# Performance work log

Measured on AMD Instinct MI355X. Metric: run time of the kernel, lower is better.

The kernel has to match this reference:

```python
import jax, jax.numpy as jnp
import numpy as np

N_NODES = 50000
N_EDGES = 1600000
IN_DIM = 128
HID = 128
N_GRAPHS = 64
N_CLASSES = 1


def _seg_sum(x, ids, n):
    return jax.ops.segment_sum(x, ids, num_segments=n)


def _gcn_layer(h, W, b, src, dst, src_isqrt, dst_isqrt):
    # DGL GraphConv, norm='both': D_dst^{-1/2} A D_src^{-1/2} (h W) + b
    hw = h @ W                                  # [N, out]
    msg = (hw * src_isqrt[:, None])[src]        # gather -> [E, out]
    agg = _seg_sum(msg, dst, h.shape[0])        # scatter-add -> [N, out]
    return agg * dst_isqrt[:, None] + b


def setup_inputs() -> dict:
    key = jax.random.key(0)
    ks = jax.random.split(key, 16)
    x = jax.random.normal(ks[0], (N_NODES, IN_DIM), dtype=jnp.float32)
    src = jax.random.randint(ks[1], (N_EDGES,), 0, N_NODES)
    dst = jax.random.randint(ks[2], (N_EDGES,), 0, N_NODES)
    graph_id = jnp.sort(jax.random.randint(ks[3], (N_NODES,), 0, N_GRAPHS))
    s = 1.0 / np.sqrt(HID)
    params = {
        'W1': jax.random.uniform(ks[4], (IN_DIM, HID), jnp.float32, -s, s),
        'b1': jnp.zeros((HID,), jnp.float32),
        'W2': jax.random.uniform(ks[5], (HID, HID), jnp.float32, -s, s),
        'b2': jnp.zeros((HID,), jnp.float32),
        'Wc1': jax.random.uniform(ks[6], (HID, HID // 2), jnp.float32, -s, s),
        'bc1': jnp.zeros((HID // 2,), jnp.float32),
        'Wc2': jax.random.uniform(ks[7], (HID // 2, HID // 4), jnp.float32, -s, s),
        'bc2': jnp.zeros((HID // 4,), jnp.float32),
        'Wc3': jax.random.uniform(ks[8], (HID // 4, HID // 8), jnp.float32, -s, s),
        'bc3': jnp.zeros((HID // 8,), jnp.float32),
        'Wc4': jax.random.uniform(ks[9], (HID // 8, N_CLASSES), jnp.float32, -s, s),
        'bc4': jnp.zeros((N_CLASSES,), jnp.float32),
    }
    return dict(x=x, src=src, dst=dst, graph_id=graph_id, num_graphs=N_GRAPHS, **params)


def reference(x, src, dst, graph_id, num_graphs, W1, b1, W2, b2,
              Wc1, bc1, Wc2, bc2, Wc3, bc3, Wc4, bc4):
    n = x.shape[0]
    ones = jnp.ones((src.shape[0],), x.dtype)
    out_deg = jnp.clip(_seg_sum(ones, src, n), 1.0)
    in_deg = jnp.clip(_seg_sum(ones, dst, n), 1.0)
    src_isqrt = jax.lax.rsqrt(out_deg)
    dst_isqrt = jax.lax.rsqrt(in_deg)

    h = jax.nn.relu(_gcn_layer(x, W1, b1, src, dst, src_isqrt, dst_isqrt))
    h = jax.nn.relu(_gcn_layer(h, W2, b2, src, dst, src_isqrt, dst_isqrt))

    # dgl.mean_nodes: per-graph mean of node features
    sums = _seg_sum(h, graph_id, num_graphs)                       # [G, HID]
    cnts = jnp.clip(_seg_sum(jnp.ones((n,), h.dtype), graph_id, num_graphs), 1.0)
    hg = sums / cnts[:, None]

    o = jax.nn.relu(hg @ Wc1 + bc1)
    o = jax.nn.relu(o @ Wc2 + bc2)
    o = jax.nn.relu(o @ Wc3 + bc3)
    return o @ Wc4 + bc4
```

## Files before the change

### kernel.cpp

```cpp
#include <hip/hip_runtime.h>
#include <hip/hip_fp16.h>

#define FDIM 128
#define NGRAPH 64
#define CBLK 256

typedef _Float16 f16;
typedef f16 f16x8 __attribute__((ext_vector_type(8)));
typedef float f32x4 __attribute__((ext_vector_type(4)));
typedef float f32x2 __attribute__((ext_vector_type(2)));

__device__ __forceinline__ int lower_bound_i(const int* a, int n, int v) {
    int lo = 0, hi = n;
    while (lo < hi) { int m = (lo + hi) >> 1; if (a[m] < v) lo = m + 1; else hi = m; }
    return lo;
}

__global__ __launch_bounds__(256) void k_pre(
        const float* __restrict__ W1, f16* __restrict__ W1h, f16* __restrict__ W1l,
        const float* __restrict__ W2, f16* __restrict__ W2h, f16* __restrict__ W2l,
        float* __restrict__ hg, const int* __restrict__ src, const int* __restrict__ dst,
        int* __restrict__ out_deg, int* __restrict__ partial,
        int E, int NBIN, int CE4) {
    __shared__ int lds[4 * 257];
    const int t = threadIdx.x;
    int b = blockIdx.x;
    if (b < 128) {
        int i = b * 256 + t;
        if (i < NGRAPH * FDIM) hg[i] = 0.f;
        int j = i & 16383;
        int k = j >> 7, n = j & 127;
        const float* W = (i < 16384) ? W1 : W2;
        f16* Wh = (i < 16384) ? W1h : W2h;
        f16* Wl = (i < 16384) ? W1l : W2l;
        float v = W[j];
        f16 hi = (f16)v;
        Wh[n * FDIM + k] = hi;
        Wl[n * FDIM + k] = (f16)(v - (float)hi);
    } else {
        b -= 128;
        for (int i = t; i < 4 * 257; i += 256) lds[i] = 0;
        __syncthreads();
        const int wv = t >> 6;
        int* hh = &lds[wv * 257];
        const int s = b * CE4, e = min(E, s + CE4);
        for (int i = s + t * 4; i < e; i += 1024) {
            if (i + 4 <= e) {
                uint4 d4 = *(const uint4*)&dst[i];
                uint4 s4 = *(const uint4*)&src[i];
                atomicAdd(&hh[d4.x >> 8], 1);
                atomicAdd(&hh[d4.y >> 8], 1);
                atomicAdd(&hh[d4.z >> 8], 1);
                atomicAdd(&hh[d4.w >> 8], 1);
                atomicAdd(&out_deg[s4.x], 1);
                atomicAdd(&out_deg[s4.y], 1);
                atomicAdd(&out_deg[s4.z], 1);
                atomicAdd(&out_deg[s4.w], 1);
            } else {
                for (int j = i; j < e; j++) {
                    atomicAdd(&hh[dst[j] >> 8], 1);
                    atomicAdd(&out_deg[src[j]], 1);
                }
            }
        }
        __syncthreads();
        for (int i = t; i < NBIN; i += 256)
            partial[i * CBLK + b] = lds[i] + lds[257 + i] + lds[514 + i] + lds[771 + i];
    }
}

__global__ __launch_bounds__(256) void k_scan(
        const int* __restrict__ partial, int* __restrict__ offs, int* __restrict__ bsum,
        int M) {
    __shared__ int lds[256];
    const int t = threadIdx.x;
    const int b = blockIdx.x;
    int i = b * 256 + t;
    int v = (i < M) ? partial[i] : 0;
    lds[t] = v;
    __syncthreads();
    for (int off = 1; off < 256; off <<= 1) {
        int x = (t >= off) ? lds[t - off] : 0;
        __syncthreads();
        lds[t] += x;
        __syncthreads();
    }
    if (i < M) offs[i] = lds[t] - v;
    if (t == 255) bsum[b] = lds[t];
}

__global__ __launch_bounds__(256) void k_coarse_scatter(
        const int* __restrict__ src, const int* __restrict__ dst,
        const int* __restrict__ offs, const int* __restrict__ bsum,
        unsigned* __restrict__ coarse_buf, int E, int CE4, int NBIN) {
    __shared__ int cur[256], sb[256];
    const int t = threadIdx.x, b = blockIdx.x;
    int v = (t < NBIN) ? bsum[t] : 0;
    sb[t] = v;
    __syncthreads();
    for (int off = 1; off < 256; off <<= 1) {
        int x = (t >= off) ? sb[t - off] : 0;
        __syncthreads();
        sb[t] += x;
        __syncthreads();
    }
    if (t < NBIN) cur[t] = offs[t * CBLK + b] + (sb[t] - v);
    __syncthreads();
    const int s = b * CE4, e = min(E, s + CE4);
    for (int i = s + t * 4; i < e; i += 1024) {
        if (i + 4 <= e) {
            uint4 d4 = *(const uint4*)&dst[i];
            uint4 s4 = *(const uint4*)&src[i];
            int p0 = atomicAdd(&cur[d4.x >> 8], 1);
            int p1 = atomicAdd(&cur[d4.y >> 8], 1);
            int p2 = atomicAdd(&cur[d4.z >> 8], 1);
            int p3 = atomicAdd(&cur[d4.w >> 8], 1);
            coarse_buf[p0] = (d4.x << 16) | s4.x;
            coarse_buf[p1] = (d4.y << 16) | s4.y;
            coarse_buf[p2] = (d4.z << 16) | s4.z;
            coarse_buf[p3] = (d4.w << 16) | s4.w;
        } else {
            for (int j = i; j < e; j++) {
                unsigned d = (unsigned)dst[j];
                int p = atomicAdd(&cur[d >> 8], 1);
                coarse_buf[p] = (d << 16) | (unsigned)src[j];
            }
        }
    }
}

template<bool IN_F16>
__device__ __forceinline__ void gemm_body(
        f16* smem, float* sisql, int blk,
        const void* __restrict__ Xv, const f16* __restrict__ Wh,
        const f16* __restrict__ Wl, const int* __restrict__ out_deg,
        float* __restrict__ sisq, unsigned char* __restrict__ out, int N) {
    const int t = threadIdx.x;
    const int w = t >> 6;
    const int lane = t & 63;
    const int base = blk * 128;

    if (t < 128) {
        int row = base + t;
        float sv = 1.f;
        if (row < N) {
            if (IN_F16) {
                sv = sisq[row];
            } else {
                sv = rsqrtf((float)max(out_deg[row], 1));
                sisq[row] = sv;
            }
        }
        sisql[t] = sv;
    }
    for (int i = t; i < 2048; i += 256) {
        int n = i >> 4, kc = (i & 15) * 8;
        *(uint4*)&smem[n * 136 + kc] = *(const uint4*)&Wh[n * FDIM + kc];
    }
    __syncthreads();

    const int mrow = lane & 15;
    const int kq = (lane >> 4) * 8;
    const int arow0 = min(base + w * 32 + mrow, N - 1);
    const int arow1 = min(base + w * 32 + 16 + mrow, N - 1);

    f16x8 a0[4], a1[4];
    if (IN_F16) {
        const f16* X = (const f16*)Xv;
#pragma unroll
        for (int kk = 0; kk < 4; kk++) {
            a0[kk] = *(const f16x8*)&X[(size_t)arow0 * FDIM + kk * 32 + kq];
            a1[kk] = *(const f16x8*)&X[(size_t)arow1 * FDIM + kk * 32 + kq];
        }
    } else {
        const float* X = (const float*)Xv;
#pragma unroll
        for (int kk = 0; kk < 4; kk++) {
            float4 u0 = *(const float4*)&X[(size_t)arow0 * FDIM + kk * 32 + kq];
            float4 u1 = *(const float4*)&X[(size_t)arow0 * FDIM + kk * 32 + kq + 4];
            float4 v0 = *(const float4*)&X[(size_t)arow1 * FDIM + kk * 32 + kq];
            float4 v1 = *(const float4*)&X[(size_t)arow1 * FDIM + kk * 32 + kq + 4];
            f16x8 av;
            av[0] = (f16)u0.x; av[1] = (f16)u0.y; av[2] = (f16)u0.z; av[3] = (f16)u0.w;
            av[4] = (f16)u1.x; av[5] = (f16)u1.y; av[6] = (f16)u1.z; av[7] = (f16)u1.w;
            a0[kk] = av;
            av[0] = (f16)v0.x; av[1] = (f16)v0.y; av[2] = (f16)v0.z; av[3] = (f16)v0.w;
            av[4] = (f16)v1.x; av[5] = (f16)v1.y; av[6] = (f16)v1.z; av[7] = (f16)v1.w;
            a1[kk] = av;
        }
    }

    f32x4 acc0[8], acc1[8];
#pragma unroll
    for (int nt = 0; nt < 8; nt++) {
        acc0[nt] = (f32x4){0.f, 0.f, 0.f, 0.f};
        acc1[nt] = (f32x4){0.f, 0.f, 0.f, 0.f};
    }

#pragma unroll
    for (int kk = 0; kk < 4; kk++) {
#pragma unroll
        for (int nt = 0; nt < 8; nt++) {
            f16x8 bh = *(const f16x8*)&smem[(nt * 16 + mrow) * 136 + kk * 32 + kq];
            f16x8 bl = *(const f16x8*)&Wl[(nt * 16 + mrow) * FDIM + kk * 32 + kq];
            acc0[nt] = __builtin_amdgcn_mfma_f32_16x16x32_f16(a0[kk], bh, acc0[nt], 0, 0, 0);
            acc1[nt] = __builtin_amdgcn_mfma_f32_16x16x32_f16(a1[kk], bh, acc1[nt], 0, 0, 0);
            acc0[nt] = __builtin_amdgcn_mfma_f32_16x16x32_f16(a0[kk], bl, acc0[nt], 0, 0, 0);
            acc1[nt] = __builtin_amdgcn_mfma_f32_16x16x32_f16(a1[kk], bl, acc1[nt], 0, 0, 0);
        }
    }

    const int r0 = (lane >> 4) * 4;
    float sv0[4], sv1[4];
#pragma unroll
    for (int j = 0; j < 4; j++) {
        sv0[j] = sisql[w * 32 + r0 + j];
        sv1[j] = sisql[w * 32 + 16 + r0 + j];
    }
    __syncthreads();
#pragma unroll
    for (int nt = 0; nt < 8; nt++) {
        int c = nt * 16 + mrow;
#pragma unroll
        for (int j = 0; j < 4; j++) {
            smem[(w * 32 + r0 + j) * 136 + c]      = (f16)(acc0[nt][j] * sv0[j]);
            smem[(w * 32 + 16 + r0 + j) * 136 + c] = (f16)(acc1[nt][j] * sv1[j]);
        }
    }
    __syncthreads();
    {
        int r = t >> 1, cb = (t & 1) * 64;
        int row = base + r;
        if (row < N) {
            unsigned char* dstp = out + (size_t)row * FDIM + cb;
#pragma unroll
            for (int g2 = 0; g2 < 4; g2++) {
                unsigned wv[4];
#pragma unroll
                for (int k2 = 0; k2 < 4; k2++) {
                    const f16* p = &smem[r * 136 + cb + g2 * 16 + k2 * 4];
                    int w0 = __builtin_amdgcn_cvt_pk_fp8_f32((float)p[0], (float)p[1], 0, false);
                    w0 = __builtin_amdgcn_cvt_pk_fp8_f32((float)p[2], (float)p[3], w0, true);
                    wv[k2] = (unsigned)w0;
                }
                uint4 u;
                u.x = wv[0]; u.y = wv[1]; u.z = wv[2]; u.w = wv[3];
                *(uint4*)&dstp[g2 * 16] = u;
            }
        }
    }
}

__global__ __launch_bounds__(256) void k_fine_gemm(
        const unsigned* __restrict__ coarse_buf, const int* __restrict__ bsum,
        int* __restrict__ csr_src, int* __restrict__ row_ptr, int N, int E, int NBIN,
        const float* __restrict__ x, const f16* __restrict__ Wh,
        const f16* __restrict__ Wl, const int* __restrict__ out_deg,
        float* __restrict__ sisq, unsigned char* __restrict__ hws) {
    __shared__ __align__(16) f16 smem[128 * 136];
    __shared__ float sisql[128];
    const int t = threadIdx.x;
    const int g = blockIdx.x;
    if (g >= NBIN) {
        gemm_body<false>(smem, sisql, g - NBIN, x, Wh, Wl, out_deg, sisq, hws, N);
        return;
    }
    int* h  = (int*)smem;
    int* sc = h + 256;
    int* cur = h + 512;
    int bv = (t < NBIN) ? bsum[t] : 0;
    sc[t] = bv;
    __syncthreads();
    for (int off = 1; off < 256; off <<= 1) {
        int xx = (t >= off) ? sc[t - off] : 0;
        __syncthreads();
        sc[t] += xx;
        __syncthreads();
    }
    __syncthreads();
    if (t == 0) { h[0] = sc[g] - bsum[g]; h[1] = sc[g]; }
    __syncthreads();
    const int s = h[0], e = h[1];
    __syncthreads();
    h[t] = 0;
    __syncthreads();
    for (int i = s + t; i < e; i += 256)
        atomicAdd(&h[(coarse_buf[i] >> 16) & 255], 1);
    __syncthreads();
    int v = h[t];
    sc[t] = v;
    __syncthreads();
    for (int off = 1; off < 256; off <<= 1) {
        int xx = (t >= off) ? sc[t - off] : 0;
        __syncthreads();
        sc[t] += xx;
        __syncthreads();
    }
    const int excl = sc[t] - v;
    const int node = g * 256 + t;
    if (node < N) row_ptr[node] = s + excl;
    if (node == N) row_ptr[N] = s + excl;
    cur[t] = s + excl;
    __syncthreads();
    for (int i = s + t; i < e; i += 256) {
        unsigned p = coarse_buf[i];
        int f = (p >> 16) & 255;
        int pos = atomicAdd(&cur[f], 1);
        csr_src[pos] = (int)(p & 0xFFFFu);
    }
    if (g == NBIN - 1 && t == 0 && (N & 255) == 0) row_ptr[N] = E;
}

__global__ __launch_bounds__(256) void k_gemm2(
        const f16* __restrict__ X, const f16* __restrict__ Wh,
        const f16* __restrict__ Wl, float* __restrict__ sisq,
        unsigned char* __restrict__ out, int N) {
    __shared__ __align__(16) f16 smem[128 * 136];
    __shared__ float sisql[128];
    gemm_body<true>(smem, sisql, blockIdx.x, X, Wh, Wl, nullptr, sisq, out, N);
}

__device__ __forceinline__ void accF8(float* acc, uint2 v) {
    f32x2 a0 = __builtin_amdgcn_cvt_pk_f32_fp8((int)v.x, false);
    f32x2 a1 = __builtin_amdgcn_cvt_pk_f32_fp8((int)v.x, true);
    f32x2 a2 = __builtin_amdgcn_cvt_pk_f32_fp8((int)v.y, false);
    f32x2 a3 = __builtin_amdgcn_cvt_pk_f32_fp8((int)v.y, true);
    acc[0] += a0.x; acc[1] += a0.y; acc[2] += a1.x; acc[3] += a1.y;
    acc[4] += a2.x; acc[5] += a2.y; acc[6] += a3.x; acc[7] += a3.y;
}

template<bool POOL>
__global__ __launch_bounds__(256) void k_aggregate(
        const unsigned char* __restrict__ hws, const int* __restrict__ csr_src,
        const int* __restrict__ row_ptr,
        const float* __restrict__ bias, f16* __restrict__ out,
        const int* __restrict__ gid, float* __restrict__ hg, int N) {
    const int t = threadIdx.x;
    const int node = blockIdx.x * 16 + (t >> 4);
    const int fbase = (t & 15) * 8;

    int s = 0, e = 0;
    if (node < N) { s = row_ptr[node]; e = row_ptr[node + 1]; }
    float acc[8];
#pragma unroll
    for (int j = 0; j < 8; j++) acc[j] = 0.f;

    int i = s;
    for (; i + 8 <= e; i += 8) {
        int u[8];
#pragma unroll
        for (int j = 0; j < 8; j++) u[j] = csr_src[i + j];
        uint2 v[8];
#pragma unroll
        for (int j = 0; j < 8; j++)
            v[j] = *(const uint2*)(hws + (size_t)u[j] * FDIM + fbase);
#pragma unroll
        for (int j = 0; j < 8; j++) accF8(acc, v[j]);
    }
    if (i + 4 <= e) {
        int u[4];
#pragma unroll
        for (int j = 0; j < 4; j++) u[j] = csr_src[i + j];
        uint2 v[4];
#pragma unroll
        for (int j = 0; j < 4; j++)
            v[j] = *(const uint2*)(hws + (size_t)u[j] * FDIM + fbase);
#pragma unroll
        for (int j = 0; j < 4; j++) accF8(acc, v[j]);
        i += 4;
    }
    for (; i < e; i++) {
        int u = csr_src[i];
        uint2 v = *(const uint2*)(hws + (size_t)u * FDIM + fbase);
        accF8(acc, v);
    }

    const float d = rsqrtf((float)max(e - s, 1));
    float res[8];
#pragma unroll
    for (int j = 0; j < 8; j++)
        res[j] = fmaxf(fmaf(acc[j], d, bias[fbase + j]), 0.f);

    if (!POOL) {
        if (node < N) {
            f16 r16[8];
#pragma unroll
            for (int j = 0; j < 8; j++) r16[j] = (f16)res[j];
            *(uint4*)(out + (size_t)node * FDIM + fbase) = *(const uint4*)r16;
        }
    } else {
        __shared__ float hgl[8 * 128];
        const int nfirst = blockIdx.x * 16;
        const int nlast = min(nfirst + 15, N - 1);
        const int g0 = gid[nfirst];
        const int span = gid[nlast] - g0 + 1;
        if (span <= 8) {
            for (int k = t; k < span * 128; k += 256) hgl[k] = 0.f;
            __syncthreads();
            if (node < N) {
                const int gg = gid[node] - g0;
#pragma unroll
                for (int j = 0; j < 8; j++)
                    atomicAdd(&hgl[gg * 128 + fbase + j], res[j]);
            }
            __syncthreads();
            for (int k = t; k < span * 128; k += 256)
                atomicAdd(&hg[g0 * 128 + k], hgl[k]);
        } else {
            if (node < N) {
                const int gg = gid[node];
#pragma unroll
                for (int j = 0; j < 8; j++)
                    atomicAdd(&hg[gg * 128 + fbase + j], res[j]);
            }
        }
    }
}

__global__ __launch_bounds__(256) void k_mlp(
        const float* __restrict__ hg, const int* __restrict__ gid, int N,
        const float* __restrict__ Wc1, const float* __restrict__ bc1,
        const float* __restrict__ Wc2, const float* __restrict__ bc2,
        const float* __restrict__ Wc3, const float* __restrict__ bc3,
        const float* __restrict__ Wc4, const float* __restrict__ bc4,
        float* __restrict__ out) {
    __shared__ float A[NGRAPH * 128];
    __shared__ float O1[NGRAPH * 64];
    __shared__ float O2[NGRAPH * 32];
    __shared__ float O3[NGRAPH * 16];
    __shared__ float inv_cnt[NGRAPH];
    const int t = threadIdx.x;

    if (t < NGRAPH) {
        int s = lower_bound_i(gid, N, t);
        int e = lower_bound_i(gid, N, t + 1);
        inv_cnt[t] = 1.f / fmaxf((float)(e - s), 1.f);
    }
    __syncthreads();

    for (int i = t; i < NGRAPH * 128; i += 256) A[i] = hg[i] * inv_cnt[i >> 7];
    __syncthreads();

    for (int i = t; i < NGRAPH * 64; i += 256) {
        int g = i >> 6, o = i & 63;
        float a = bc1[o];
        for (int k = 0; k < 128; k++) a = fmaf(A[g * 128 + k], Wc1[k * 64 + o], a);
        O1[i] = fmaxf(a, 0.f);
    }
    __syncthreads();

    for (int i = t; i < NGRAPH * 32; i += 256) {
        int g = i >> 5, o = i & 31;
        float a = bc2[o];
        for (int k = 0; k < 64; k++) a = fmaf(O1[g * 64 + k], Wc2[k * 32 + o], a);
        O2[i] = fmaxf(a, 0.f);
    }
    __syncthreads();

    for (int i = t; i < NGRAPH * 16; i += 256) {
        int g = i >> 4, o = i & 15;
        float a = bc3[o];
        for (int k = 0; k < 32; k++) a = fmaf(O2[g * 32 + k], Wc3[k * 16 + o], a);
        O3[i] = fmaxf(a, 0.f);
    }
    __syncthreads();

    if (t < NGRAPH) {
        float a = bc4[0];
        for (int k = 0; k < 16; k++) a = fmaf(O3[t * 16 + k], Wc4[k], a);
        out[t] = a;
    }
}

extern "C" void kernel_launch(void* const* d_in, const int* in_sizes, int n_in,
                              void* d_out, int out_size, void* d_ws, size_t ws_size,
                              hipStream_t stream) {
    const float* x   = (const float*)d_in[0];
    const int*   src = (const int*)d_in[1];
    const int*   dst = (const int*)d_in[2];
    const int*   gid = (const int*)d_in[3];
    const float* W1  = (const float*)d_in[5];
    const float* b1  = (const float*)d_in[6];
    const float* W2  = (const float*)d_in[7];
    const float* b2  = (const float*)d_in[8];
    const float* Wc1 = (const float*)d_in[9];
    const float* bc1 = (const float*)d_in[10];
    const float* Wc2 = (const float*)d_in[11];
    const float* bc2 = (const float*)d_in[12];
    const float* Wc3 = (const float*)d_in[13];
    const float* bc3 = (const float*)d_in[14];
    const float* Wc4 = (const float*)d_in[15];
    const float* bc4 = (const float*)d_in[16];
    float* out = (float*)d_out;

    const int N = in_sizes[0] / FDIM;
    const int E = in_sizes[1];

    const int NBIN = (N + 255) >> 8;
    const int M    = NBIN * CBLK;
    const int CE4  = (((E + CBLK - 1) / CBLK) + 3) & ~3;

    char* w = (char*)d_ws;
    size_t off = 0;
    auto alloc = [&](size_t bytes) -> void* {
        void* p = w + off;
        off = (off + bytes + 255) & ~(size_t)255;
        return p;
    };
    unsigned char* hws = (unsigned char*)alloc((size_t)N * FDIM);
    f16*   h       = (f16*)   alloc((size_t)N * FDIM * 2);
    int*   csr_src = (int*)   alloc((size_t)E * 4);
    unsigned* coarse_buf = (unsigned*)alloc((size_t)E * 4);
    int*   out_deg = (int*)   alloc((size_t)N * 4);
    int*   partial = (int*)   alloc((size_t)M * 4);
    int*   offs    = (int*)   alloc((size_t)M * 4);
    int*   row_ptr = (int*)   alloc((size_t)(N + 1) * 4);
    float* sisq    = (float*) alloc((size_t)N * 4);
    int*   bsum    = (int*)   alloc(256 * 4);
    float* hg      = (float*) alloc(NGRAPH * FDIM * 4);
    f16*   W1t     = (f16*)   alloc(FDIM * FDIM * 2);
    f16*   W1l     = (f16*)   alloc(FDIM * FDIM * 2);
    f16*   W2t     = (f16*)   alloc(FDIM * FDIM * 2);
    f16*   W2l     = (f16*)   alloc(FDIM * FDIM * 2);

    const int gT = (N + 127) / 128;
    const int gA = (N + 15) / 16;

    hipMemsetAsync(out_deg, 0, (size_t)N * 4, stream);
    k_pre<<<128 + CBLK, 256, 0, stream>>>(
        W1, W1t, W1l, W2, W2t, W2l, hg, src, dst, out_deg, partial, E, NBIN, CE4);
    k_scan<<<NBIN, 256, 0, stream>>>(partial, offs, bsum, M);
    k_coarse_scatter<<<CBLK, 256, 0, stream>>>(src, dst, offs, bsum, coarse_buf, E, CE4, NBIN);
    k_fine_gemm<<<NBIN + gT, 256, 0, stream>>>(
        coarse_buf, bsum, csr_src, row_ptr, N, E, NBIN,
        x, W1t, W1l, out_deg, sisq, hws);
    k_aggregate<false><<<gA, 256, 0, stream>>>(hws, csr_src, row_ptr, b1, h, nullptr, nullptr, N);
    k_gemm2<<<gT, 256, 0, stream>>>(h, W2t, W2l, sisq, hws, N);
    k_aggregate<true><<<gA, 256, 0, stream>>>(hws, csr_src, row_ptr, b2, nullptr, gid, hg, N);
    k_mlp<<<1, 256, 0, stream>>>(hg, gid, N, Wc1, bc1, Wc2, bc2, Wc3, bc3, Wc4, bc4, out);
}
```

Measured before the change: 341.8 us.

## Compute out-degrees with LDS-privatized packed 16-bit histograms instead of global atomics

Replaces the global atomicAdd out-degree count with per-block LDS histograms. Each histogram covers a chunk of nodes and packs two 16-bit counters per word, and each edge slice writes a partial array to global memory. The scan kernel gets extra blocks that reduce the 64 partials per node and write the rsqrt normalization, so the GEMM no longer computes it and the memset goes away. The aim is to remove contended global atomics, at the cost of extra blocks that re-read src once per node chunk and a 64xN/2 partial buffer. 16-bit counters could overflow if a slice holds more than 65535 edges from one node.

```diff
diff --git a/kernel.cpp b/kernel.cpp
--- a/kernel.cpp
+++ b/kernel.cpp
@@ -4,6 +4,8 @@
 #define FDIM 128
 #define NGRAPH 64
 #define CBLK 256
+#define OCH2 12800
+#define OSL 64
 
 typedef _Float16 f16;
 typedef f16 f16x8 __attribute__((ext_vector_type(8)));
@@ -20,9 +22,9 @@
         const float* __restrict__ W1, f16* __restrict__ W1h, f16* __restrict__ W1l,
         const float* __restrict__ W2, f16* __restrict__ W2h, f16* __restrict__ W2l,
         float* __restrict__ hg, const int* __restrict__ src, const int* __restrict__ dst,
-        int* __restrict__ out_deg, int* __restrict__ partial,
-        int E, int NBIN, int CE4) {
-    __shared__ int lds[4 * 257];
+        unsigned* __restrict__ od_part, int* __restrict__ partial,
+        int E, int NBIN, int CE4, int NH) {
+    __shared__ __align__(16) unsigned shmem_u[OCH2];
     const int t = threadIdx.x;
     int b = blockIdx.x;
     if (b < 128) {
@@ -37,8 +39,9 @@
         f16 hi = (f16)v;
         Wh[n * FDIM + k] = hi;
         Wl[n * FDIM + k] = (f16)(v - (float)hi);
-    } else {
+    } else if (b < 128 + CBLK) {
         b -= 128;
+        int* lds = (int*)shmem_u;
         for (int i = t; i < 4 * 257; i += 256) lds[i] = 0;
         __syncthreads();
         const int wv = t >> 6;
@@ -47,46 +50,91 @@
         for (int i = s + t * 4; i < e; i += 1024) {
             if (i + 4 <= e) {
                 uint4 d4 = *(const uint4*)&dst[i];
-                uint4 s4 = *(const uint4*)&src[i];
                 atomicAdd(&hh[d4.x >> 8], 1);
                 atomicAdd(&hh[d4.y >> 8], 1);
                 atomicAdd(&hh[d4.z >> 8], 1);
                 atomicAdd(&hh[d4.w >> 8], 1);
-                atomicAdd(&out_deg[s4.x], 1);
-                atomicAdd(&out_deg[s4.y], 1);
-                atomicAdd(&out_deg[s4.z], 1);
-                atomicAdd(&out_deg[s4.w], 1);
+            } else {
+                for (int j = i; j < e; j++) atomicAdd(&hh[dst[j] >> 8], 1);
+            }
+        }
+        __syncthreads();
+        for (int i = t; i < NBIN; i += 256)
+            partial[i * CBLK + b] = lds[i] + lds[257 + i] + lds[514 + i] + lds[771 + i];
+    } else {
+        const int ob = b - 128 - CBLK;
+        const int c  = ob >> 6;
+        const int sl = ob & (OSL - 1);
+        for (int i = t; i < OCH2; i += 256) shmem_u[i] = 0u;
+        __syncthreads();
+        const int plo = c * OCH2;
+        const int vlo = plo * 2;
+        const int SE = (((E + OSL - 1) / OSL) + 3) & ~3;
+        const int s = sl * SE, e = min(E, s + SE);
+        for (int i = s + t * 4; i < e; i += 1024) {
+            if (i + 4 <= e) {
+                uint4 s4 = *(const uint4*)&src[i];
+                int v0 = (int)s4.x - vlo, v1 = (int)s4.y - vlo;
+                int v2 = (int)s4.z - vlo, v3 = (int)s4.w - vlo;
+                if ((unsigned)v0 < (unsigned)(2 * OCH2))
+                    atomicAdd(&shmem_u[v0 >> 1], 1u << ((v0 & 1) * 16));
+                if ((unsigned)v1 < (unsigned)(2 * OCH2))
+                    atomicAdd(&shmem_u[v1 >> 1], 1u << ((v1 & 1) * 16));
+                if ((unsigned)v2 < (unsigned)(2 * OCH2))
+                    atomicAdd(&shmem_u[v2 >> 1], 1u << ((v2 & 1) * 16));
+                if ((unsigned)v3 < (unsigned)(2 * OCH2))
+                    atomicAdd(&shmem_u[v3 >> 1], 1u << ((v3 & 1) * 16));
             } else {
                 for (int j = i; j < e; j++) {
-                    atomicAdd(&hh[dst[j] >> 8], 1);
-                    atomicAdd(&out_deg[src[j]], 1);
+                    int v = src[j] - vlo;
+                    if ((unsigned)v < (unsigned)(2 * OCH2))
+                        atomicAdd(&shmem_u[v >> 1], 1u << ((v & 1) * 16));
                 }
             }
         }
         __syncthreads();
-        for (int i = t; i < NBIN; i += 256)
-            partial[i * CBLK + b] = lds[i] + lds[257 + i] + lds[514 + i] + lds[771 + i];
+        const int hiN = min(NH - plo, OCH2);
+        for (int i = t; i < hiN; i += 256)
+            od_part[(size_t)sl * NH + plo + i] = shmem_u[i];
     }
 }
 
 __global__ __launch_bounds__(256) void k_scan(
         const int* __restrict__ partial, int* __restrict__ offs, int* __restrict__ bsum,
-        int M) {
+        int M, const unsigned* __restrict__ od_part, float* __restrict__ sisq,
+        int NH, int N, int NBIN) {
     __shared__ int lds[256];
     const int t = threadIdx.x;
-    const int b = blockIdx.x;
-    int i = b * 256 + t;
-    int v = (i < M) ? partial[i] : 0;
-    lds[t] = v;
-    __syncthreads();
-    for (int off = 1; off < 256; off <<= 1) {
-        int x = (t >= off) ? lds[t - off] : 0;
-        __syncthreads();
-        lds[t] += x;
-        __syncthreads();
-    }
-    if (i < M) offs[i] = lds[t] - v;
-    if (t == 255) bsum[b] = lds[t];
+    int b = blockIdx.x;
+    if (b < NBIN) {
+        int i = b * 256 + t;
+        int v = (i < M) ? partial[i] : 0;
+        lds[t] = v;
+        __syncthreads();
+        for (int off = 1; off < 256; off <<= 1) {
+            int x = (t >= off) ? lds[t - off] : 0;
+            __syncthreads();
+            lds[t] += x;
+            __syncthreads();
+        }
+        if (i < M) offs[i] = lds[t] - v;
+        if (t == 255) bsum[b] = lds[t];
+    } else {
+        b -= NBIN;
+        const int i = b * 256 + t;
+        if (i < NH) {
+            unsigned lo = 0, hi = 0;
+#pragma unroll 8
+            for (int s = 0; s < OSL; s++) {
+                unsigned v = od_part[(size_t)s * NH + i];
+                lo += v & 0xFFFFu;
+                hi += v >> 16;
+            }
+            const int n0 = 2 * i, n1 = 2 * i + 1;
+            sisq[n0] = rsqrtf((float)max((int)lo, 1));
+            if (n1 < N) sisq[n1] = rsqrtf((float)max((int)hi, 1));
+        }
+    }
 }
 
 __global__ __launch_bounds__(256) void k_coarse_scatter(
@@ -133,8 +181,8 @@
 __device__ __forceinline__ void gemm_body(
         f16* smem, float* sisql, int blk,
         const void* __restrict__ Xv, const f16* __restrict__ Wh,
-        const f16* __restrict__ Wl, const int* __restrict__ out_deg,
-        float* __restrict__ sisq, unsigned char* __restrict__ out, int N) {
+        const f16* __restrict__ Wl, const float* __restrict__ sisq,
+        unsigned char* __restrict__ out, int N) {
     const int t = threadIdx.x;
     const int w = t >> 6;
     const int lane = t & 63;
@@ -142,16 +190,7 @@
 
     if (t < 128) {
         int row = base + t;
-        float sv = 1.f;
-        if (row < N) {
-            if (IN_F16) {
-                sv = sisq[row];
-            } else {
-                sv = rsqrtf((float)max(out_deg[row], 1));
-                sisq[row] = sv;
-            }
-        }
-        sisql[t] = sv;
+        sisql[t] = (row < N) ? sisq[row] : 1.f;
     }
     for (int i = t; i < 2048; i += 256) {
         int n = i >> 4, kc = (i & 15) * 8;
@@ -255,14 +294,14 @@
         const unsigned* __restrict__ coarse_buf, const int* __restrict__ bsum,
         int* __restrict__ csr_src, int* __restrict__ row_ptr, int N, int E, int NBIN,
         const float* __restrict__ x, const f16* __restrict__ Wh,
-        const f16* __restrict__ Wl, const int* __restrict__ out_deg,
-        float* __restrict__ sisq, unsigned char* __restrict__ hws) {
+        const f16* __restrict__ Wl, const float* __restrict__ sisq,
+        unsigned char* __restrict__ hws) {
     __shared__ __align__(16) f16 smem[128 * 136];
     __shared__ float sisql[128];
     const int t = threadIdx.x;
     const int g = blockIdx.x;
     if (g >= NBIN) {
-        gemm_body<false>(smem, sisql, g - NBIN, x, Wh, Wl, out_deg, sisq, hws, N);
+        gemm_body<false>(smem, sisql, g - NBIN, x, Wh, Wl, sisq, hws, N);
         return;
     }
     int* h  = (int*)smem;
@@ -313,11 +352,11 @@
 
 __global__ __launch_bounds__(256) void k_gemm2(
         const f16* __restrict__ X, const f16* __restrict__ Wh,
-        const f16* __restrict__ Wl, float* __restrict__ sisq,
+        const f16* __restrict__ Wl, const float* __restrict__ sisq,
         unsigned char* __restrict__ out, int N) {
     __shared__ __align__(16) f16 smem[128 * 136];
     __shared__ float sisql[128];
-    gemm_body<true>(smem, sisql, blockIdx.x, X, Wh, Wl, nullptr, sisq, out, N);
+    gemm_body<true>(smem, sisql, blockIdx.x, X, Wh, Wl, sisq, out, N);
 }
 
 __device__ __forceinline__ void accF8(float* acc, uint2 v) {
@@ -499,6 +538,9 @@
     const int NBIN = (N + 255) >> 8;
     const int M    = NBIN * CBLK;
     const int CE4  = (((E + CBLK - 1) / CBLK) + 3) & ~3;
+    const int NH   = (N + 1) >> 1;
+    const int OC2  = (NH + OCH2 - 1) / OCH2;
+    const int MB   = (NH + 255) >> 8;
 
     char* w = (char*)d_ws;
     size_t off = 0;
@@ -511,7 +553,7 @@
     f16*   h       = (f16*)   alloc((size_t)N * FDIM * 2);
     int*   csr_src = (int*)   alloc((size_t)E * 4);
     unsigned* coarse_buf = (unsigned*)alloc((size_t)E * 4);
-    int*   out_deg = (int*)   alloc((size_t)N * 4);
+    unsigned* od_part = (unsigned*)alloc((size_t)OSL * NH * 4);
     int*   partial = (int*)   alloc((size_t)M * 4);
     int*   offs    = (int*)   alloc((size_t)M * 4);
     int*   row_ptr = (int*)   alloc((size_t)(N + 1) * 4);
@@ -526,14 +568,13 @@
     const int gT = (N + 127) / 128;
     const int gA = (N + 15) / 16;
 
-    hipMemsetAsync(out_deg, 0, (size_t)N * 4, stream);
-    k_pre<<<128 + CBLK, 256, 0, stream>>>(
-        W1, W1t, W1l, W2, W2t, W2l, hg, src, dst, out_deg, partial, E, NBIN, CE4);
-    k_scan<<<NBIN, 256, 0, stream>>>(partial, offs, bsum, M);
+    k_pre<<<128 + CBLK + OC2 * OSL, 256, 0, stream>>>(
+        W1, W1t, W1l, W2, W2t, W2l, hg, src, dst, od_part, partial, E, NBIN, CE4, NH);
+    k_scan<<<NBIN + MB, 256, 0, stream>>>(partial, offs, bsum, M, od_part, sisq, NH, N, NBIN);
     k_coarse_scatter<<<CBLK, 256, 0, stream>>>(src, dst, offs, bsum, coarse_buf, E, CE4, NBIN);
     k_fine_gemm<<<NBIN + gT, 256, 0, stream>>>(
         coarse_buf, bsum, csr_src, row_ptr, N, E, NBIN,
-        x, W1t, W1l, out_deg, sisq, hws);
+        x, W1t, W1l, sisq, hws);
     k_aggregate<false><<<gA, 256, 0, stream>>>(hws, csr_src, row_ptr, b1, h, nullptr, nullptr, N);
     k_gemm2<<<gT, 256, 0, stream>>>(h, W2t, W2l, sisq, hws, N);
     k_aggregate<true><<<gA, 256, 0, stream>>>(hws, csr_src, row_ptr, b2, nullptr, gid, hg, N);
```

Result: faster. 284.9 us (-16.6%).
